# Performance work log

Measured on AMD Instinct MI355X. Metric: run time of the kernel, lower is better.

The kernel has to match this reference:

```python
import jax, jax.numpy as jnp
import numpy as np

IN_DIM = 14400
K = 25
DIMS = [7200, 3600, 1800]  # floor(in_dim / 2**(i+1))
OUT_DIM = 2
BATCH = 256


def setup_inputs() -> dict:
    key = jax.random.key(0)
    ks = jax.random.split(key, 32)
    inp = {}
    inp["x"] = jax.random.normal(ks[0], (BATCH, 2 * IN_DIM), dtype=jnp.float32)
    # shared KNN tables (both channels load the same h5 files)
    prev = [IN_DIM] + DIMS[:-1]
    for i, (d, p) in enumerate(zip(DIMS, prev)):
        inp[f"knn{i}"] = jax.random.randint(ks[1 + i], (d, K), 0, p, dtype=jnp.int64)
    std = (2.0 / K) ** 0.5
    kidx = 4
    for ch in ("p", "n"):
        for i, d in enumerate(DIMS):
            inp[f"w{ch}{i}"] = jax.random.normal(ks[kidx], (d, K), dtype=jnp.float32) * std; kidx += 1
            inp[f"b{ch}{i}"] = jnp.zeros((1, d), dtype=jnp.float32)
        inp[f"fc{ch}_w"] = jax.random.normal(ks[kidx], (OUT_DIM, DIMS[-1]), dtype=jnp.float32) * (1.0 / DIMS[-1] ** 0.5); kidx += 1
        inp[f"fc{ch}_b"] = jnp.zeros((OUT_DIM,), dtype=jnp.float32)
    inp["fc3_w"] = jax.random.normal(ks[kidx], (OUT_DIM, 4), dtype=jnp.float32) * 0.5
    inp["fc3_b"] = jnp.zeros((OUT_DIM,), dtype=jnp.float32)
    return inp


def _lcn(x, knns, ws, bs, fw, fb):
    # x: (B, in_dim). Each layer: gather KNN neighbors, weighted sum, bias, relu.
    for knn, w, b in zip(knns, ws, bs):
        g = x[:, knn]                                  # (B, dim, K) gather
        x = jax.nn.relu(jnp.einsum('bdk,dk->bd', g, w) + b)
    return x @ fw.T + fb                               # fc_angle


def reference(x, knn0, knn1, knn2,
              wp0, bp0, wp1, bp1, wp2, bp2, fcp_w, fcp_b,
              wn0, bn0, wn1, bn1, wn2, bn2, fcn_w, fcn_b,
              fc3_w, fc3_b):
    knns = (knn0, knn1, knn2)
    xpos = _lcn(x[:, :IN_DIM], knns, (wp0, wp1, wp2), (bp0, bp1, bp2), fcp_w, fcp_b)
    xneg = _lcn(x[:, IN_DIM:], knns, (wn0, wn1, wn2), (bn0, bn1, bn2), fcn_w, fcn_b)
    h = jax.nn.relu(jnp.concatenate([xpos, xneg], axis=1))  # (B, 4)
    return h @ fc3_w.T + fc3_b
```

## Files before the change

### kernel.cpp

```cpp
#include <hip/hip_runtime.h>
#include <hip/hip_bf16.h>

using bf16 = __hip_bfloat16;

#define K 25
#define D0 7200
#define D1 3600
#define D2 1800

#define PKB_L1 360000
#define PKB_L2 540000
#define NPK    630000
#define NPB    25200

#define NT 1024

__device__ __forceinline__ float b2f(ushort u) {
  unsigned int w = ((unsigned int)u) << 16;
  float f; __builtin_memcpy(&f, &w, 4); return f;
}
__device__ __forceinline__ ushort f2b(float f) {
  bf16 h = __float2bfloat16(f);
  ushort u; __builtin_memcpy(&u, &h, 2); return u;
}

__global__ __launch_bounds__(256) void prepack_kernel(
    const void* __restrict__ x,
    const void* __restrict__ knn0, const void* __restrict__ knn1,
    const void* __restrict__ knn2,
    const void* __restrict__ wp0, const void* __restrict__ bp0,
    const void* __restrict__ wp1, const void* __restrict__ bp1,
    const void* __restrict__ wp2, const void* __restrict__ bp2,
    const void* __restrict__ wn0, const void* __restrict__ bn0,
    const void* __restrict__ wn1, const void* __restrict__ bn1,
    const void* __restrict__ wn2, const void* __restrict__ bn2,
    unsigned int* __restrict__ pk, float* __restrict__ pbias,
    float* __restrict__ y, int* __restrict__ flags) {
  __shared__ int s_flags[2];
  const int t = threadIdx.x;
  if (t < 64) {
    const unsigned int u = ((const unsigned int*)x)[t * 997];
    const unsigned int e = (u >> 23) & 0xFF;
    const unsigned long long m = __ballot((e >= 192) || (e <= 30));
    if (t == 0) s_flags[0] = (__popcll(m) >= 32) ? 1 : 0;
  } else if (t < 128) {
    const int l = t - 64;
    const unsigned int hi = ((const unsigned int*)knn0)[2 * l + 1];
    const unsigned long long m = __ballot(hi != 0);
    if (l == 0) s_flags[1] = (m == 0ULL) ? 1 : 0;
  }
  __syncthreads();
  const int fdt = s_flags[0], idt = s_flags[1];

  if (blockIdx.x == 0 && t == 0) {
    flags[0] = fdt; flags[1] = idt; flags[16] = 0;
  }

  const int gid = blockIdx.x * 256 + t;
  if (gid < NPB) {
    int i = gid, d, dout, pkb;
    const void *kn, *wsel, *bsel;
    if (i < 14400) {
      const int ch = i / D0; d = i - ch * D0; dout = D0;
      pkb = ch * 180000; kn = knn0;
      wsel = ch ? wn0 : wp0; bsel = ch ? bn0 : bp0;
    } else if (i < 21600) {
      i -= 14400; const int ch = i / D1; d = i - ch * D1; dout = D1;
      pkb = PKB_L1 + ch * 90000; kn = knn1;
      wsel = ch ? wn1 : wp1; bsel = ch ? bn1 : bp1;
    } else {
      i -= 21600; const int ch = i / D2; d = i - ch * D2; dout = D2;
      pkb = PKB_L2 + ch * 45000; kn = knn2;
      wsel = ch ? wn2 : wp2; bsel = ch ? bn2 : bp2;
    }
    const int pos0 = d * K;
#pragma unroll
    for (int k = 0; k < K; ++k) {
      const unsigned int idx = idt ? ((const unsigned int*)kn)[2 * (pos0 + k)]
                                   : ((const unsigned int*)kn)[pos0 + k];
      const ushort wb = fdt ? ((const ushort*)wsel)[pos0 + k]
                            : f2b(((const float*)wsel)[pos0 + k]);
      pk[pkb + k * dout + d] = (idx << 16) | (unsigned int)wb;
    }
    pbias[gid] = fdt ? b2f(((const ushort*)bsel)[d]) : ((const float*)bsel)[d];
  } else if (gid < NPB + 1024) {
    y[gid - NPB] = 0.0f;
  }
}

__device__ __forceinline__ void layer_run(ushort* lds, const unsigned int* __restrict__ pk,
                                          const float* __restrict__ pbias,
                                          int offIn, int offOut, int pkb, int pbb,
                                          int dout) {
  for (int d = threadIdx.x; d < dout; d += NT) {
    const unsigned int* s = pk + pkb + d;
    float a0 = 0.f, a1 = 0.f;
#pragma unroll
    for (int k = 0; k < K; ++k) {
      const unsigned int pw = s[k * dout];
      const unsigned int vv = *(const unsigned int*)&lds[offIn + ((pw >> 16) << 1)];
      const float w = b2f((ushort)(pw & 0xFFFFu));
      a0 = fmaf(w, b2f((ushort)(vv & 0xFFFFu)), a0);
      a1 = fmaf(w, b2f((ushort)(vv >> 16)), a1);
    }
    const float bias = pbias[pbb + d];
    a0 = fmaxf(a0 + bias, 0.f);
    a1 = fmaxf(a1 + bias, 0.f);
    *(unsigned int*)&lds[offOut + (d << 1)] =
        (unsigned int)f2b(a0) | ((unsigned int)f2b(a1) << 16);
  }
}

__global__ __launch_bounds__(NT) void lcn_fused(
    const void* __restrict__ x, const unsigned int* __restrict__ pk,
    const float* __restrict__ pbias,
    const void* __restrict__ fcpw, const void* __restrict__ fcnw,
    const void* __restrict__ fcpb, const void* __restrict__ fcnb,
    const void* __restrict__ f3w, const void* __restrict__ f3b,
    float* __restrict__ y, int* __restrict__ flags, void* __restrict__ out) {
  __shared__ ushort lds[43200];
  __shared__ float red[NT / 64][4];
  __shared__ int sflag;
  const int t = threadIdx.x;
  const int ch = blockIdx.x & 1;
  const int b0 = (blockIdx.x >> 1) * 2;

  if (t == 0) sflag = flags[0];
  __syncthreads();
  const int fdt = sflag;

  if (fdt) {
    const ushort* r0 = (const ushort*)x + (size_t)b0 * 28800 + ch * 14400;
    const ushort* r1 = r0 + 28800;
    for (int c = t; c < 3600; c += NT) {
      const ushort4 a = ((const ushort4*)r0)[c];
      const ushort4 b = ((const ushort4*)r1)[c];
      unsigned int* dst = (unsigned int*)&lds[c * 8];
      dst[0] = (unsigned int)a.x | ((unsigned int)b.x << 16);
      dst[1] = (unsigned int)a.y | ((unsigned int)b.y << 16);
      dst[2] = (unsigned int)a.z | ((unsigned int)b.z << 16);
      dst[3] = (unsigned int)a.w | ((unsigned int)b.w << 16);
    }
  } else {
    const float* r0 = (const float*)x + (size_t)b0 * 28800 + ch * 14400;
    const float* r1 = r0 + 28800;
    for (int c = t; c < 3600; c += NT) {
      const float4 a = ((const float4*)r0)[c];
      const float4 b = ((const float4*)r1)[c];
      unsigned int* dst = (unsigned int*)&lds[c * 8];
      dst[0] = (unsigned int)f2b(a.x) | ((unsigned int)f2b(b.x) << 16);
      dst[1] = (unsigned int)f2b(a.y) | ((unsigned int)f2b(b.y) << 16);
      dst[2] = (unsigned int)f2b(a.z) | ((unsigned int)f2b(b.z) << 16);
      dst[3] = (unsigned int)f2b(a.w) | ((unsigned int)f2b(b.w) << 16);
    }
  }
  __syncthreads();

  layer_run(lds, pk, pbias, 0, 28800, 0 + ch * 180000, 0 + ch * D0, D0);
  __syncthreads();
  layer_run(lds, pk, pbias, 28800, 0, PKB_L1 + ch * 90000, 14400 + ch * D1, D1);
  __syncthreads();
  layer_run(lds, pk, pbias, 0, 7200, PKB_L2 + ch * 45000, 21600 + ch * D2, D2);
  __syncthreads();

  {
    const void* fw = ch ? fcnw : fcpw;
    float a00 = 0.f, a01 = 0.f, a10 = 0.f, a11 = 0.f;
    for (int d = t; d < D2; d += NT) {
      const unsigned int vv = *(const unsigned int*)&lds[7200 + (d << 1)];
      const float v0 = b2f((ushort)(vv & 0xFFFFu));
      const float v1 = b2f((ushort)(vv >> 16));
      const float w0 = fdt ? b2f(((const ushort*)fw)[d]) : ((const float*)fw)[d];
      const float w1 = fdt ? b2f(((const ushort*)fw)[D2 + d]) : ((const float*)fw)[D2 + d];
      a00 = fmaf(w0, v0, a00); a01 = fmaf(w0, v1, a01);
      a10 = fmaf(w1, v0, a10); a11 = fmaf(w1, v1, a11);
    }
#pragma unroll
    for (int off = 32; off > 0; off >>= 1) {
      a00 += __shfl_down(a00, off);
      a01 += __shfl_down(a01, off);
      a10 += __shfl_down(a10, off);
      a11 += __shfl_down(a11, off);
    }
    const int wave = t >> 6, lane = t & 63;
    if (lane == 0) {
      red[wave][0] = a00; red[wave][1] = a01; red[wave][2] = a10; red[wave][3] = a11;
    }
    __syncthreads();
    if (t == 0) {
      float s00 = 0.f, s01 = 0.f, s10 = 0.f, s11 = 0.f;
#pragma unroll
      for (int wv = 0; wv < NT / 64; ++wv) {
        s00 += red[wv][0]; s01 += red[wv][1]; s10 += red[wv][2]; s11 += red[wv][3];
      }
      atomicAdd(&y[(ch * 2 + 0) * 256 + b0], s00);
      atomicAdd(&y[(ch * 2 + 0) * 256 + b0 + 1], s01);
      atomicAdd(&y[(ch * 2 + 1) * 256 + b0], s10);
      atomicAdd(&y[(ch * 2 + 1) * 256 + b0 + 1], s11);
    }
  }

  __syncthreads();
  if (t == 0) {
    __threadfence();
    sflag = (atomicAdd(&flags[16], 1) == (int)gridDim.x - 1) ? 1 : 0;
  }
  __syncthreads();
  if (sflag && t < 256) {
    const int b = t;
    const float y0 = atomicAdd(&y[0 * 256 + b], 0.0f);
    const float y1 = atomicAdd(&y[1 * 256 + b], 0.0f);
    const float y2 = atomicAdd(&y[2 * 256 + b], 0.0f);
    const float y3 = atomicAdd(&y[3 * 256 + b], 0.0f);
    const float bp0v = fdt ? b2f(((const ushort*)fcpb)[0]) : ((const float*)fcpb)[0];
    const float bp1v = fdt ? b2f(((const ushort*)fcpb)[1]) : ((const float*)fcpb)[1];
    const float bn0v = fdt ? b2f(((const ushort*)fcnb)[0]) : ((const float*)fcnb)[0];
    const float bn1v = fdt ? b2f(((const ushort*)fcnb)[1]) : ((const float*)fcnb)[1];
    const float h0v = fmaxf(y0 + bp0v, 0.f);
    const float h1v = fmaxf(y1 + bp1v, 0.f);
    const float h2v = fmaxf(y2 + bn0v, 0.f);
    const float h3v = fmaxf(y3 + bn1v, 0.f);
#pragma unroll
    for (int o = 0; o < 2; ++o) {
      float w0, w1, w2, w3, bb;
      if (fdt) {
        const ushort* fp = (const ushort*)f3w;
        w0 = b2f(fp[o * 4 + 0]); w1 = b2f(fp[o * 4 + 1]);
        w2 = b2f(fp[o * 4 + 2]); w3 = b2f(fp[o * 4 + 3]);
        bb = b2f(((const ushort*)f3b)[o]);
      } else {
        const float* fp = (const float*)f3w;
        w0 = fp[o * 4 + 0]; w1 = fp[o * 4 + 1];
        w2 = fp[o * 4 + 2]; w3 = fp[o * 4 + 3];
        bb = ((const float*)f3b)[o];
      }
      float r = bb;
      r = fmaf(w0, h0v, r); r = fmaf(w1, h1v, r);
      r = fmaf(w2, h2v, r); r = fmaf(w3, h3v, r);
      if (fdt) ((ushort*)out)[b * 2 + o] = f2b(r);
      else     ((float*)out)[b * 2 + o] = r;
    }
  }
}

extern "C" void kernel_launch(void* const* d_in, const int* in_sizes, int n_in,
                              void* d_out, int out_size, void* d_ws, size_t ws_size,
                              hipStream_t stream) {
  const void* x    = d_in[0];
  const void* knn0 = d_in[1];
  const void* knn1 = d_in[2];
  const void* knn2 = d_in[3];
  const void* wp0  = d_in[4];  const void* bp0 = d_in[5];
  const void* wp1  = d_in[6];  const void* bp1 = d_in[7];
  const void* wp2  = d_in[8];  const void* bp2 = d_in[9];
  const void* fcpw = d_in[10]; const void* fcpb = d_in[11];
  const void* wn0  = d_in[12]; const void* bn0 = d_in[13];
  const void* wn1  = d_in[14]; const void* bn1 = d_in[15];
  const void* wn2  = d_in[16]; const void* bn2 = d_in[17];
  const void* fcnw = d_in[18]; const void* fcnb = d_in[19];
  const void* f3w  = d_in[20]; const void* f3b  = d_in[21];

  char* ws = (char*)d_ws;
  unsigned int* pk = (unsigned int*)(ws);
  float* pbias = (float*)(ws + 2520000);
  float* y     = (float*)(ws + 2620800);
  int* flags   = (int*)(ws + 2624896);

  prepack_kernel<<<103, 256, 0, stream>>>(x, knn0, knn1, knn2,
                                          wp0, bp0, wp1, bp1, wp2, bp2,
                                          wn0, bn0, wn1, bn1, wn2, bn2,
                                          pk, pbias, y, flags);

  lcn_fused<<<256, NT, 0, stream>>>(x, pk, pbias, fcpw, fcnw, fcpb, fcnb,
                                    f3w, f3b, y, flags, d_out);
}
```

Baseline: 147.8 us.

## Stage prepack reads through LDS and process two outputs per thread in layers

The prepack kernel now assigns each block a 256-row tile of one layer/channel and loads its KNN indices and weights into shared memory with coalesced reads before writing the packed transposed table. Previously each thread read 25 strided elements directly, which made global loads uncoalesced. The layer loop in the fused kernel also handles two output positions per thread per iteration, giving more independent loads and FMAs in flight at the cost of extra registers. The prepack grid grows by one block to match the new tiling.

```diff
diff --git a/kernel.cpp b/kernel.cpp
--- a/kernel.cpp
+++ b/kernel.cpp
@@ -10,8 +10,6 @@
 
 #define PKB_L1 360000
 #define PKB_L2 540000
-#define NPK    630000
-#define NPB    25200
 
 #define NT 1024
 
@@ -36,8 +34,11 @@
     const void* __restrict__ wn2, const void* __restrict__ bn2,
     unsigned int* __restrict__ pk, float* __restrict__ pbias,
     float* __restrict__ y, int* __restrict__ flags) {
+  __shared__ unsigned int s_idx[6400];
+  __shared__ ushort s_w[6400];
   __shared__ int s_flags[2];
   const int t = threadIdx.x;
+
   if (t < 64) {
     const unsigned int u = ((const unsigned int*)x)[t * 997];
     const unsigned int e = (u >> 23) & 0xFF;
@@ -55,36 +56,49 @@
   if (blockIdx.x == 0 && t == 0) {
     flags[0] = fdt; flags[1] = idt; flags[16] = 0;
   }
-
-  const int gid = blockIdx.x * 256 + t;
-  if (gid < NPB) {
-    int i = gid, d, dout, pkb;
-    const void *kn, *wsel, *bsel;
-    if (i < 14400) {
-      const int ch = i / D0; d = i - ch * D0; dout = D0;
-      pkb = ch * 180000; kn = knn0;
-      wsel = ch ? wn0 : wp0; bsel = ch ? bn0 : bp0;
-    } else if (i < 21600) {
-      i -= 14400; const int ch = i / D1; d = i - ch * D1; dout = D1;
-      pkb = PKB_L1 + ch * 90000; kn = knn1;
-      wsel = ch ? wn1 : wp1; bsel = ch ? bn1 : bp1;
-    } else {
-      i -= 21600; const int ch = i / D2; d = i - ch * D2; dout = D2;
-      pkb = PKB_L2 + ch * 45000; kn = knn2;
-      wsel = ch ? wn2 : wp2; bsel = ch ? bn2 : bp2;
-    }
-    const int pos0 = d * K;
+  if (blockIdx.x < 4) y[blockIdx.x * 256 + t] = 0.0f;
+
+  int bb = (int)blockIdx.x, dout, pkb, pbase, d0;
+  const void *kn, *wsel, *bsel;
+  if (bb < 58) {
+    const int ch = bb >= 29; const int lb = ch ? bb - 29 : bb;
+    dout = D0; kn = knn0; pkb = ch ? 180000 : 0; pbase = ch ? 7200 : 0;
+    wsel = ch ? wn0 : wp0; bsel = ch ? bn0 : bp0; d0 = lb * 256;
+  } else if (bb < 88) {
+    bb -= 58; const int ch = bb >= 15; const int lb = ch ? bb - 15 : bb;
+    dout = D1; kn = knn1; pkb = PKB_L1 + ch * 90000; pbase = 14400 + ch * D1;
+    wsel = ch ? wn1 : wp1; bsel = ch ? bn1 : bp1; d0 = lb * 256;
+  } else {
+    bb -= 88; const int ch = bb >= 8; const int lb = ch ? bb - 8 : bb;
+    dout = D2; kn = knn2; pkb = PKB_L2 + ch * 45000; pbase = 21600 + ch * D2;
+    wsel = ch ? wn2 : wp2; bsel = ch ? bn2 : bp2; d0 = lb * 256;
+  }
+  const int cnt = min(256, dout - d0);
+  const int n = cnt * K;
+
+  if (idt) {
+    const uint2* src = (const uint2*)kn + (size_t)d0 * K;
+    for (int i = t; i < n; i += 256) s_idx[i] = src[i].x;
+  } else {
+    const unsigned int* src = (const unsigned int*)kn + (size_t)d0 * K;
+    for (int i = t; i < n; i += 256) s_idx[i] = src[i];
+  }
+  if (fdt) {
+    const ushort* src = (const ushort*)wsel + (size_t)d0 * K;
+    for (int i = t; i < n; i += 256) s_w[i] = src[i];
+  } else {
+    const float* src = (const float*)wsel + (size_t)d0 * K;
+    for (int i = t; i < n; i += 256) s_w[i] = f2b(src[i]);
+  }
+  __syncthreads();
+
+  if (t < cnt) {
+    const int d = d0 + t;
 #pragma unroll
     for (int k = 0; k < K; ++k) {
-      const unsigned int idx = idt ? ((const unsigned int*)kn)[2 * (pos0 + k)]
-                                   : ((const unsigned int*)kn)[pos0 + k];
-      const ushort wb = fdt ? ((const ushort*)wsel)[pos0 + k]
-                            : f2b(((const float*)wsel)[pos0 + k]);
-      pk[pkb + k * dout + d] = (idx << 16) | (unsigned int)wb;
-    }
-    pbias[gid] = fdt ? b2f(((const ushort*)bsel)[d]) : ((const float*)bsel)[d];
-  } else if (gid < NPB + 1024) {
-    y[gid - NPB] = 0.0f;
+      pk[pkb + k * dout + d] = (s_idx[t * K + k] << 16) | (unsigned int)s_w[t * K + k];
+    }
+    pbias[pbase + d] = fdt ? b2f(((const ushort*)bsel)[d]) : ((const float*)bsel)[d];
   }
 }
 
@@ -92,7 +106,34 @@
                                           const float* __restrict__ pbias,
                                           int offIn, int offOut, int pkb, int pbb,
                                           int dout) {
-  for (int d = threadIdx.x; d < dout; d += NT) {
+  int d = threadIdx.x;
+  for (; d + NT < dout; d += 2 * NT) {
+    const unsigned int* s0 = pk + pkb + d;
+    const unsigned int* s1 = s0 + NT;
+    float a0 = 0.f, a1 = 0.f, c0 = 0.f, c1 = 0.f;
+#pragma unroll
+    for (int k = 0; k < K; ++k) {
+      const unsigned int pw0 = s0[k * dout];
+      const unsigned int pw1 = s1[k * dout];
+      const unsigned int vv0 = *(const unsigned int*)&lds[offIn + ((pw0 >> 16) << 1)];
+      const unsigned int vv1 = *(const unsigned int*)&lds[offIn + ((pw1 >> 16) << 1)];
+      const float w0 = b2f((ushort)(pw0 & 0xFFFFu));
+      const float w1 = b2f((ushort)(pw1 & 0xFFFFu));
+      a0 = fmaf(w0, b2f((ushort)(vv0 & 0xFFFFu)), a0);
+      a1 = fmaf(w0, b2f((ushort)(vv0 >> 16)), a1);
+      c0 = fmaf(w1, b2f((ushort)(vv1 & 0xFFFFu)), c0);
+      c1 = fmaf(w1, b2f((ushort)(vv1 >> 16)), c1);
+    }
+    const float bias0 = pbias[pbb + d];
+    const float bias1 = pbias[pbb + d + NT];
+    a0 = fmaxf(a0 + bias0, 0.f); a1 = fmaxf(a1 + bias0, 0.f);
+    c0 = fmaxf(c0 + bias1, 0.f); c1 = fmaxf(c1 + bias1, 0.f);
+    *(unsigned int*)&lds[offOut + (d << 1)] =
+        (unsigned int)f2b(a0) | ((unsigned int)f2b(a1) << 16);
+    *(unsigned int*)&lds[offOut + ((d + NT) << 1)] =
+        (unsigned int)f2b(c0) | ((unsigned int)f2b(c1) << 16);
+  }
+  if (d < dout) {
     const unsigned int* s = pk + pkb + d;
     float a0 = 0.f, a1 = 0.f;
 #pragma unroll
@@ -266,7 +307,7 @@
   float* y     = (float*)(ws + 2620800);
   int* flags   = (int*)(ws + 2624896);
 
-  prepack_kernel<<<103, 256, 0, stream>>>(x, knn0, knn1, knn2,
+  prepack_kernel<<<104, 256, 0, stream>>>(x, knn0, knn1, knn2,
                                           wp0, bp0, wp1, bp1, wp2, bp2,
                                           wn0, bn0, wn1, bn1, wn2, bn2,
                                           pk, pbias, y, flags);
```

Result: slower. 180.5 us (+22.1%).
